# Optimization experiments

Measured on AMD Instinct MI355X. Metric: run time of the kernel, lower is better.

## Reference

```python
import jax, jax.numpy as jnp
import numpy as np
from jax import lax

B, T, C_IN, C_OUT, H = 2048, 128, 2, 16, 232


def setup_inputs() -> dict:
    key = jax.random.key(0)
    k0, k1, k2, k3 = jax.random.split(key, 4)
    X = jax.random.normal(k0, (B, T, C_IN), dtype=jnp.float32)
    # kaiming_normal init (fan_in mode) as in reset_parameters
    conv_w = jax.random.normal(k1, (C_OUT, C_IN, 3), dtype=jnp.float32) * np.sqrt(2.0 / (C_IN * 3))
    conv_b = jnp.zeros((C_OUT,), dtype=jnp.float32)
    w_ih = jax.random.normal(k2, (3 * H, C_OUT), dtype=jnp.float32) * np.sqrt(2.0 / C_OUT)
    w_hh = jax.random.normal(k3, (3 * H, H), dtype=jnp.float32) * np.sqrt(2.0 / H)
    b_ih = jnp.zeros((3 * H,), dtype=jnp.float32)
    b_hh = jnp.zeros((3 * H,), dtype=jnp.float32)
    return {"X": X, "conv_w": conv_w, "conv_b": conv_b,
            "w_ih": w_ih, "w_hh": w_hh, "b_ih": b_ih, "b_hh": b_hh}


def reference(X, conv_w, conv_b, w_ih, w_hh, b_ih, b_hh):
    # Conv1d(2->16, k=3, pad=1) on [B, C, T] + ReLU
    Xc = jnp.transpose(X, (0, 2, 1))                      # [B, 2, T]
    y = lax.conv_general_dilated(Xc, conv_w, window_strides=(1,),
                                 padding=[(1, 1)],
                                 dimension_numbers=("NCH", "OIH", "NCH"))
    y = jax.nn.relu(y + conv_b[None, :, None])            # [B, 16, T]
    x_embed = jnp.transpose(y, (0, 2, 1))                 # [B, T, 16]

    # GRU (torch gate order: r, z, n). Precompute input projections for all t.
    gi = jnp.einsum("btc,gc->btg", x_embed, w_ih) + b_ih  # [B, T, 3H]

    def step(h, g_t):
        gh = h @ w_hh.T + b_hh                            # [B, 3H]
        ir, iz, in_ = jnp.split(g_t, 3, axis=-1)
        hr, hz, hn = jnp.split(gh, 3, axis=-1)
        r = jax.nn.sigmoid(ir + hr)
        z = jax.nn.sigmoid(iz + hz)
        n = jnp.tanh(in_ + r * hn)
        h_new = (1.0 - z) * n + z * h
        return h_new, None

    h0 = jnp.zeros((X.shape[0], w_hh.shape[1]), dtype=X.dtype)
    hT, _ = lax.scan(step, h0, jnp.moveaxis(gi, 1, 0))    # final state [B, H]
    return hT
```

## Files before the change

kernel.cpp:

```cpp
#include <hip/hip_runtime.h>

#define BATCH 2048
#define T     128
#define CIN   2
#define COUT  16
#define H     232
#define RPB   8
#define NBLK  (BATCH/RPB)
#define NTHR  512
#define NGRP  15
#define NT2   48
#define NS    9
#define HROW  272
#define HBUF_H (RPB * HROW)

#define OFF_HA   0
#define SZ_HA    (2 * RPB * HROW * 2)
#define OFF_XE   (OFF_HA + SZ_HA)
#define SZ_XE    (T * RPB * 16 * 2)
#define OFF_WL   (OFF_XE + SZ_XE)
#define SZ_WL    (8 * 14 * 64 * 8 * 2)
#define OFF_CW   (OFF_WL + SZ_WL)
#define SZ_CW    512
#define SMEM_BYTES (OFF_CW + SZ_CW)
#define OFF_XE_H (OFF_XE / 2)

typedef _Float16 half8 __attribute__((ext_vector_type(8)));
typedef float  floatx4 __attribute__((ext_vector_type(4)));

#define MFMA __builtin_amdgcn_mfma_f32_16x16x32_f16

__device__ __align__(16) _Float16 g_packedW[NT2 * NS * 64 * 8];

__global__ void pack_w_kernel(const float* __restrict__ w_ih,
                              const float* __restrict__ w_hh) {
  int tile = blockIdx.x, slice = blockIdx.y, lane = threadIdx.x;
  int grp = tile / NGRP;
  int j   = (tile % NGRP) * 16 + (lane & 15);
  int g   = grp * H + j;
  bool valid = (tile < 3 * NGRP) && (j < H);
  half8 v = {};
  if (valid) {
#pragma unroll
    for (int i = 0; i < 8; ++i) {
      int k = slice * 32 + ((lane >> 4) << 3) + i;
      float f = 0.f;
      if (slice < 8) {
        if (k < H) f = w_hh[g * H + k];
        else if (k < H + COUT && grp < 2) f = w_ih[g * COUT + (k - H)];
      } else {
        int xk = k - 256;
        if (xk >= 0 && xk < COUT && grp == 2) f = w_ih[g * COUT + xk];
      }
      v[i] = (_Float16)f;
    }
  }
  *(half8*)&g_packedW[((tile * NS + slice) * 64 + lane) * 8] = v;
}

__device__ __forceinline__ float sigmoid_f(float x) {
  return __builtin_amdgcn_rcpf(1.f + __expf(-x));
}

__global__ __launch_bounds__(NTHR, 2) void st_gru_kernel(
    const float* __restrict__ X,
    const float* __restrict__ conv_w, const float* __restrict__ conv_b,
    const float* __restrict__ b_ih, const float* __restrict__ b_hh,
    float* __restrict__ out) {

  extern __shared__ __align__(16) char smem[];
  _Float16* lds16  = (_Float16*)smem;
  _Float16* hAflat = (_Float16*)(smem + OFF_HA);
  _Float16* Xemb   = (_Float16*)(smem + OFF_XE);
  _Float16* wLDS   = (_Float16*)(smem + OFF_WL);
  float*    cwp    = (float*)(smem + OFF_CW);

  const int tid  = threadIdx.x;
  const int lane = tid & 63;
  const int wave = tid >> 6;
  const int r_a  = lane & 15;
  const int ch4  = lane >> 4;
  const int blk  = blockIdx.x;
  const int rr   = r_a & 7;
  const int swz  = rr & 3;

  for (int i = tid; i < 2 * RPB * HROW; i += NTHR) hAflat[i] = (_Float16)0;
  if (tid < COUT * CIN * 3) cwp[tid] = conv_w[tid];
  if (tid < COUT) cwp[96 + tid] = conv_b[tid];
  __syncthreads();

  for (int p = tid; p < RPB * T; p += NTHR) {
    int r = p >> 7, t = p & (T - 1);
    const float* xr = X + (size_t)(blk * RPB + r) * (T * CIN);
    float x0[3], x1[3];
#pragma unroll
    for (int d = 0; d < 3; ++d) {
      int tt = t + d - 1;
      bool ok = (unsigned)tt < (unsigned)T;
      x0[d] = ok ? xr[tt * 2] : 0.f;
      x1[d] = ok ? xr[tt * 2 + 1] : 0.f;
    }
    half8 lo, hi;
#pragma unroll
    for (int c = 0; c < COUT; ++c) {
      float a = cwp[96 + c];
#pragma unroll
      for (int d = 0; d < 3; ++d)
        a += x0[d] * cwp[c * 6 + d] + x1[d] * cwp[c * 6 + 3 + d];
      _Float16 hv = (_Float16)fmaxf(a, 0.f);
      if (c < 8) lo[c] = hv; else hi[c - 8] = hv;
    }
    *(half8*)&Xemb[(t * RPB + r) * 16] = lo;
    *(half8*)&Xemb[(t * RPB + r) * 16 + 8] = hi;
  }

  const int gi0 = wave * 2, gi1 = wave * 2 + 1;
  const bool g1ok = (gi1 < NGRP);
  const int tr0 = gi0, tz0 = gi0 + NGRP, tn0 = gi0 + 2 * NGRP;
  const int tr1 = g1ok ? gi1 : 45, tz1 = g1ok ? gi1 + NGRP : 46, tn1 = g1ok ? gi1 + 2 * NGRP : 47;
  const half8* Wp = (const half8*)g_packedW;

  half8* myz = (half8*)(wLDS + wave * (14 * 64 * 8));
#pragma unroll
  for (int f = 0; f < 6; ++f) myz[f * 64 + lane] = Wp[(tz0 * NS + f) * 64 + lane];
#pragma unroll
  for (int f = 0; f < 6; ++f) myz[(6 + f) * 64 + lane] = Wp[(tz1 * NS + f) * 64 + lane];
  myz[12 * 64 + lane] = Wp[(tn0 * NS + 8) * 64 + lane];
  myz[13 * 64 + lane] = Wp[(tn1 * NS + 8) * 64 + lane];

  half8 wr0[8], wr1[8], wn0[8], wn1[8], wzh0[2], wzh1[2];
#pragma unroll
  for (int s = 0; s < 8; ++s) {
    wr0[s] = Wp[(tr0 * NS + s) * 64 + lane];
    wr1[s] = Wp[(tr1 * NS + s) * 64 + lane];
    wn0[s] = Wp[(tn0 * NS + s) * 64 + lane];
    wn1[s] = Wp[(tn1 * NS + s) * 64 + lane];
  }
  wzh0[0] = Wp[(tz0 * NS + 6) * 64 + lane];
  wzh0[1] = Wp[(tz0 * NS + 7) * 64 + lane];
  wzh1[0] = Wp[(tz1 * NS + 6) * 64 + lane];
  wzh1[1] = Wp[(tz1 * NS + 7) * 64 + lane];

  const int j0 = gi0 * 16 + r_a, j1 = gi1 * 16 + r_a;
  float bsr0 = 0.f, bsz0 = 0.f, bin0 = 0.f, bhn0 = 0.f;
  float bsr1 = 0.f, bsz1 = 0.f, bin1 = 0.f, bhn1 = 0.f;
  if (j0 < H) {
    bsr0 = b_ih[j0] + b_hh[j0];
    bsz0 = b_ih[H + j0] + b_hh[H + j0];
    bin0 = b_ih[2 * H + j0]; bhn0 = b_hh[2 * H + j0];
  }
  if (g1ok && j1 < H) {
    bsr1 = b_ih[j1] + b_hh[j1];
    bsz1 = b_ih[H + j1] + b_hh[H + j1];
    bin1 = b_ih[2 * H + j1]; bhn1 = b_hh[2 * H + j1];
  }

  const int eb   = (ch4 & 2);
  const int rowb = ((ch4 & 1) << 2) | (ch4 & 2);

  int woff0[2], woff1[2];
#pragma unroll
  for (int u = 0; u < 2; ++u) {
    int row = rowb + u;
    woff0[u] = row * HROW + ((j0 & ~31) | ((((j0 >> 3) & 3) ^ (row & 3)) << 3) | (j0 & 7));
    woff1[u] = row * HROW + ((j1 & ~31) | ((((j1 >> 3) & 3) ^ (row & 3)) << 3) | (j1 & 7));
  }

  float h0[2] = {0.f, 0.f};
  float h1[2] = {0.f, 0.f};

  const int aoff = rr * HROW + ((ch4 ^ swz) << 3);
  const int inc7 = (ch4 == 0) ? 0 : 256;
  int pa7_e = (ch4 == 0) ? (0      + rr * HROW + 224 + (swz << 3))
                         : (OFF_XE_H + rr * 16 + ((ch4 == 2) ? 8 : 0));
  int pa7_o = (ch4 == 0) ? (HBUF_H + rr * HROW + 224 + (swz << 3))
                         : (OFF_XE_H + 128 + rr * 16 + ((ch4 == 2) ? 8 : 0));
  int a8i = OFF_XE_H + rr * 16 + ((ch4 & 1) << 3);

  __syncthreads();

#define GRU_STEP(RBH, WBH, PA7, A8I) do {                                      \
    half8 A_[7];                                                               \
    _Pragma("unroll")                                                          \
    for (int s = 0; s < 7; ++s)                                                \
      A_[s] = *(const half8*)&lds16[(RBH) + aoff + s * 32];                    \
    half8 A7_ = *(const half8*)&lds16[(PA7)];                                  \
    half8 A8_ = *(const half8*)&lds16[(A8I)];                                  \
    floatx4 ra0 = {}, za0 = {}, na0 = {}, xa0 = {};                            \
    _Pragma("unroll")                                                          \
    for (int s = 0; s < 6; ++s) {                                              \
      ra0 = MFMA(A_[s], wr0[s], ra0, 0, 0, 0);                                 \
      za0 = MFMA(A_[s], myz[s * 64 + lane], za0, 0, 0, 0);                     \
      na0 = MFMA(A_[s], wn0[s], na0, 0, 0, 0);                                 \
    }                                                                          \
    ra0 = MFMA(A_[6], wr0[6], ra0, 0, 0, 0);                                   \
    za0 = MFMA(A_[6], wzh0[0], za0, 0, 0, 0);                                  \
    na0 = MFMA(A_[6], wn0[6], na0, 0, 0, 0);                                   \
    ra0 = MFMA(A7_, wr0[7], ra0, 0, 0, 0);                                     \
    za0 = MFMA(A7_, wzh0[1], za0, 0, 0, 0);                                    \
    na0 = MFMA(A7_, wn0[7], na0, 0, 0, 0);                                     \
    xa0 = MFMA(A8_, myz[12 * 64 + lane], xa0, 0, 0, 0);                        \
    if (g1ok) {                                                                \
      floatx4 ra1 = {}, za1 = {}, na1 = {}, xa1 = {};                          \
      _Pragma("unroll")                                                        \
      for (int s = 0; s < 4; ++s) {                                            \
        ra1 = MFMA(A_[s], wr1[s], ra1, 0, 0, 0);                               \
        za1 = MFMA(A_[s], myz[(6 + s) * 64 + lane], za1, 0, 0, 0);             \
        na1 = MFMA(A_[s], wn1[s], na1, 0, 0, 0);                               \
      }                                                                        \
      float sr_[2], sz_[2];                                                    \
      _Pragma("unroll")                                                        \
      for (int u = 0; u < 2; ++u) {                                            \
        sr_[u] = sigmoid_f(ra0[eb + u] + bsr0);                                \
        sz_[u] = sigmoid_f(za0[eb + u] + bsz0);                                \
      }                                                                        \
      _Pragma("unroll")                                                        \
      for (int s = 4; s < 6; ++s) {                                            \
        ra1 = MFMA(A_[s], wr1[s], ra1, 0, 0, 0);                               \
        za1 = MFMA(A_[s], myz[(6 + s) * 64 + lane], za1, 0, 0, 0);             \
        na1 = MFMA(A_[s], wn1[s], na1, 0, 0, 0);                               \
      }                                                                        \
      ra1 = MFMA(A_[6], wr1[6], ra1, 0, 0, 0);                                 \
      za1 = MFMA(A_[6], wzh1[0], za1, 0, 0, 0);                                \
      na1 = MFMA(A_[6], wn1[6], na1, 0, 0, 0);                                 \
      _Pragma("unroll")                                                        \
      for (int u = 0; u < 2; ++u) {                                            \
        float pre = xa0[eb + u] + bin0 + sr_[u] * (na0[eb + u] + bhn0);        \
        float ee = __expf(2.f * pre);                                          \
        float n = 1.f - 2.f * __builtin_amdgcn_rcpf(ee + 1.f);                 \
        h0[u] = n + sz_[u] * (h0[u] - n);                                      \
        lds16[(WBH) + woff0[u]] = (_Float16)h0[u];                             \
      }                                                                        \
      ra1 = MFMA(A7_, wr1[7], ra1, 0, 0, 0);                                   \
      za1 = MFMA(A7_, wzh1[1], za1, 0, 0, 0);                                  \
      na1 = MFMA(A7_, wn1[7], na1, 0, 0, 0);                                   \
      xa1 = MFMA(A8_, myz[13 * 64 + lane], xa1, 0, 0, 0);                      \
      _Pragma("unroll")                                                        \
      for (int u = 0; u < 2; ++u) {                                            \
        float r = sigmoid_f(ra1[eb + u] + bsr1);                               \
        float z = sigmoid_f(za1[eb + u] + bsz1);                               \
        float pre = xa1[eb + u] + bin1 + r * (na1[eb + u] + bhn1);             \
        float ee = __expf(2.f * pre);                                          \
        float n = 1.f - 2.f * __builtin_amdgcn_rcpf(ee + 1.f);                 \
        h1[u] = n + z * (h1[u] - n);                                           \
        lds16[(WBH) + woff1[u]] = (_Float16)h1[u];                             \
      }                                                                        \
    } else {                                                                   \
      _Pragma("unroll")                                                        \
      for (int u = 0; u < 2; ++u) {                                            \
        float r = sigmoid_f(ra0[eb + u] + bsr0);                               \
        float z = sigmoid_f(za0[eb + u] + bsz0);                               \
        float pre = xa0[eb + u] + bin0 + r * (na0[eb + u] + bhn0);             \
        float ee = __expf(2.f * pre);                                          \
        float n = 1.f - 2.f * __builtin_amdgcn_rcpf(ee + 1.f);                 \
        h0[u] = n + z * (h0[u] - n);                                           \
        lds16[(WBH) + woff0[u]] = (_Float16)h0[u];                             \
      }                                                                        \
    }                                                                          \
    __syncthreads();                                                           \
  } while (0)

  for (int tt = 0; tt < T; tt += 2) {
    GRU_STEP(0,      HBUF_H, pa7_e, a8i);
    GRU_STEP(HBUF_H, 0,      pa7_o, a8i + 128);
    pa7_e += inc7; pa7_o += inc7; a8i += 256;
  }
#undef GRU_STEP

#pragma unroll
  for (int u = 0; u < 2; ++u) {
    int row = rowb + u;
    if (j0 < H) out[(size_t)(blk * RPB + row) * H + j0] = h0[u];
    if (g1ok && j1 < H) out[(size_t)(blk * RPB + row) * H + j1] = h1[u];
  }
}

extern "C" void kernel_launch(void* const* d_in, const int* in_sizes, int n_in,
                              void* d_out, int out_size, void* d_ws, size_t ws_size,
                              hipStream_t stream) {
  const float* X      = (const float*)d_in[0];
  const float* conv_w = (const float*)d_in[1];
  const float* conv_b = (const float*)d_in[2];
  const float* w_ih   = (const float*)d_in[3];
  const float* w_hh   = (const float*)d_in[4];
  const float* b_ih   = (const float*)d_in[5];
  const float* b_hh   = (const float*)d_in[6];
  float* out = (float*)d_out;

  static bool attr_set = false;
  if (!attr_set) {
    hipFuncSetAttribute((const void*)st_gru_kernel,
                        hipFuncAttributeMaxDynamicSharedMemorySize, SMEM_BYTES);
    attr_set = true;
  }

  pack_w_kernel<<<dim3(NT2, NS), 64, 0, stream>>>(w_ih, w_hh);
  st_gru_kernel<<<NBLK, NTHR, SMEM_BYTES, stream>>>(X, conv_w, conv_b, b_ih, b_hh, out);
}
```

Baseline: 185.7 us.

## Reorder GRU step MFMAs into phases and use exp2-based gate activations

```diff
diff --git a/kernel.cpp b/kernel.cpp
--- a/kernel.cpp
+++ b/kernel.cpp
@@ -25,10 +25,14 @@
 #define SMEM_BYTES (OFF_CW + SZ_CW)
 #define OFF_XE_H (OFF_XE / 2)
 
+#define L2E   1.4426950408889634f
+#define TWO_L2E 2.8853900817779268f
+
 typedef _Float16 half8 __attribute__((ext_vector_type(8)));
 typedef float  floatx4 __attribute__((ext_vector_type(4)));
 
 #define MFMA __builtin_amdgcn_mfma_f32_16x16x32_f16
+#define SBAR0() __builtin_amdgcn_sched_barrier(0)
 
 __device__ __align__(16) _Float16 g_packedW[NT2 * NS * 64 * 8];
 
@@ -58,10 +62,6 @@
   *(half8*)&g_packedW[((tile * NS + slice) * 64 + lane) * 8] = v;
 }
 
-__device__ __forceinline__ float sigmoid_f(float x) {
-  return __builtin_amdgcn_rcpf(1.f + __expf(-x));
-}
-
 __global__ __launch_bounds__(NTHR, 2) void st_gru_kernel(
     const float* __restrict__ X,
     const float* __restrict__ conv_w, const float* __restrict__ conv_b,
@@ -142,16 +142,16 @@
   wzh1[1] = Wp[(tz1 * NS + 7) * 64 + lane];
 
   const int j0 = gi0 * 16 + r_a, j1 = gi1 * 16 + r_a;
-  float bsr0 = 0.f, bsz0 = 0.f, bin0 = 0.f, bhn0 = 0.f;
-  float bsr1 = 0.f, bsz1 = 0.f, bin1 = 0.f, bhn1 = 0.f;
+  float nbsr0 = 0.f, nbsz0 = 0.f, bin0 = 0.f, bhn0 = 0.f;
+  float nbsr1 = 0.f, nbsz1 = 0.f, bin1 = 0.f, bhn1 = 0.f;
   if (j0 < H) {
-    bsr0 = b_ih[j0] + b_hh[j0];
-    bsz0 = b_ih[H + j0] + b_hh[H + j0];
+    nbsr0 = -L2E * (b_ih[j0] + b_hh[j0]);
+    nbsz0 = -L2E * (b_ih[H + j0] + b_hh[H + j0]);
     bin0 = b_ih[2 * H + j0]; bhn0 = b_hh[2 * H + j0];
   }
   if (g1ok && j1 < H) {
-    bsr1 = b_ih[j1] + b_hh[j1];
-    bsz1 = b_ih[H + j1] + b_hh[H + j1];
+    nbsr1 = -L2E * (b_ih[j1] + b_hh[j1]);
+    nbsz1 = -L2E * (b_ih[H + j1] + b_hh[H + j1]);
     bin1 = b_ih[2 * H + j1]; bhn1 = b_hh[2 * H + j1];
   }
 
@@ -186,75 +186,72 @@
       A_[s] = *(const half8*)&lds16[(RBH) + aoff + s * 32];                    \
     half8 A7_ = *(const half8*)&lds16[(PA7)];                                  \
     half8 A8_ = *(const half8*)&lds16[(A8I)];                                  \
-    floatx4 ra0 = {}, za0 = {}, na0 = {}, xa0 = {};                            \
-    _Pragma("unroll")                                                          \
-    for (int s = 0; s < 6; ++s) {                                              \
+      \
+    floatx4 ra0 = {}, na0 = {}, za0 = {}, ra1 = {}, na1 = {}, za1 = {};        \
+    _Pragma("unroll")                                                          \
+    for (int s = 0; s < 7; ++s) {                                              \
       ra0 = MFMA(A_[s], wr0[s], ra0, 0, 0, 0);                                 \
-      za0 = MFMA(A_[s], myz[s * 64 + lane], za0, 0, 0, 0);                     \
       na0 = MFMA(A_[s], wn0[s], na0, 0, 0, 0);                                 \
-    }                                                                          \
-    ra0 = MFMA(A_[6], wr0[6], ra0, 0, 0, 0);                                   \
-    za0 = MFMA(A_[6], wzh0[0], za0, 0, 0, 0);                                  \
-    na0 = MFMA(A_[6], wn0[6], na0, 0, 0, 0);                                   \
-    ra0 = MFMA(A7_, wr0[7], ra0, 0, 0, 0);                                     \
-    za0 = MFMA(A7_, wzh0[1], za0, 0, 0, 0);                                    \
-    na0 = MFMA(A7_, wn0[7], na0, 0, 0, 0);                                     \
-    xa0 = MFMA(A8_, myz[12 * 64 + lane], xa0, 0, 0, 0);                        \
-    if (g1ok) {                                                                \
-      floatx4 ra1 = {}, za1 = {}, na1 = {}, xa1 = {};                          \
-      _Pragma("unroll")                                                        \
-      for (int s = 0; s < 4; ++s) {                                            \
+      if (g1ok) {                                                              \
         ra1 = MFMA(A_[s], wr1[s], ra1, 0, 0, 0);                               \
-        za1 = MFMA(A_[s], myz[(6 + s) * 64 + lane], za1, 0, 0, 0);             \
         na1 = MFMA(A_[s], wn1[s], na1, 0, 0, 0);                               \
       }                                                                        \
-      float sr_[2], sz_[2];                                                    \
+    }                                                                          \
+    za0 = MFMA(A_[6], wzh0[0], za0, 0, 0, 0);                                  \
+    za0 = MFMA(A7_, wzh0[1], za0, 0, 0, 0);                                    \
+    ra0 = MFMA(A7_, wr0[7], ra0, 0, 0, 0);                                     \
+    na0 = MFMA(A7_, wn0[7], na0, 0, 0, 0);                                     \
+    if (g1ok) {                                                                \
+      za1 = MFMA(A_[6], wzh1[0], za1, 0, 0, 0);                                \
+      za1 = MFMA(A7_, wzh1[1], za1, 0, 0, 0);                                  \
+      ra1 = MFMA(A7_, wr1[7], ra1, 0, 0, 0);                                   \
+      na1 = MFMA(A7_, wn1[7], na1, 0, 0, 0);                                   \
+    }                                                                          \
+       \
+    float sr0_[2], sr1_[2];                                                    \
+    _Pragma("unroll")                                                          \
+    for (int u = 0; u < 2; ++u) {                                              \
+      sr0_[u] = __builtin_amdgcn_rcpf(                                         \
+          1.f + __builtin_amdgcn_exp2f(fmaf(ra0[eb + u], -L2E, nbsr0)));       \
+      sr1_[u] = __builtin_amdgcn_rcpf(                                         \
+          1.f + __builtin_amdgcn_exp2f(fmaf(ra1[eb + u], -L2E, nbsr1)));       \
+    }                                                                          \
+    SBAR0();                                                                   \
+                        \
+    floatx4 xa0 = {};                                                          \
+    _Pragma("unroll")                                                          \
+    for (int s = 0; s < 6; ++s)                                                \
+      za0 = MFMA(A_[s], myz[s * 64 + lane], za0, 0, 0, 0);                     \
+    xa0 = MFMA(A8_, myz[12 * 64 + lane], xa0, 0, 0, 0);                        \
+                                   \
+    _Pragma("unroll")                                                          \
+    for (int u = 0; u < 2; ++u) {                                              \
+      float sz = __builtin_amdgcn_rcpf(                                        \
+          1.f + __builtin_amdgcn_exp2f(fmaf(za0[eb + u], -L2E, nbsz0)));       \
+      float pre = fmaf(sr0_[u], na0[eb + u] + bhn0, xa0[eb + u] + bin0);       \
+      float e2 = __builtin_amdgcn_exp2f(pre * TWO_L2E);                        \
+      float n = fmaf(-2.f, __builtin_amdgcn_rcpf(e2 + 1.f), 1.f);              \
+      h0[u] = fmaf(sz, h0[u] - n, n);                                          \
+      lds16[(WBH) + woff0[u]] = (_Float16)h0[u];                               \
+    }                                                                          \
+    SBAR0();                                                                   \
+                        \
+    if (g1ok) {                                                                \
+      floatx4 xa1 = {};                                                        \
+      _Pragma("unroll")                                                        \
+      for (int s = 0; s < 6; ++s)                                              \
+        za1 = MFMA(A_[s], myz[(6 + s) * 64 + lane], za1, 0, 0, 0);             \
+      xa1 = MFMA(A8_, myz[13 * 64 + lane], xa1, 0, 0, 0);                      \
+                                          \
       _Pragma("unroll")                                                        \
       for (int u = 0; u < 2; ++u) {                                            \
-        sr_[u] = sigmoid_f(ra0[eb + u] + bsr0);                                \
-        sz_[u] = sigmoid_f(za0[eb + u] + bsz0);                                \
-      }                                                                        \
-      _Pragma("unroll")                                                        \
-      for (int s = 4; s < 6; ++s) {                                            \
-        ra1 = MFMA(A_[s], wr1[s], ra1, 0, 0, 0);                               \
-        za1 = MFMA(A_[s], myz[(6 + s) * 64 + lane], za1, 0, 0, 0);             \
-        na1 = MFMA(A_[s], wn1[s], na1, 0, 0, 0);                               \
-      }                                                                        \
-      ra1 = MFMA(A_[6], wr1[6], ra1, 0, 0, 0);                                 \
-      za1 = MFMA(A_[6], wzh1[0], za1, 0, 0, 0);                                \
-      na1 = MFMA(A_[6], wn1[6], na1, 0, 0, 0);                                 \
-      _Pragma("unroll")                                                        \
-      for (int u = 0; u < 2; ++u) {                                            \
-        float pre = xa0[eb + u] + bin0 + sr_[u] * (na0[eb + u] + bhn0);        \
-        float ee = __expf(2.f * pre);                                          \
-        float n = 1.f - 2.f * __builtin_amdgcn_rcpf(ee + 1.f);                 \
-        h0[u] = n + sz_[u] * (h0[u] - n);                                      \
-        lds16[(WBH) + woff0[u]] = (_Float16)h0[u];                             \
-      }                                                                        \
-      ra1 = MFMA(A7_, wr1[7], ra1, 0, 0, 0);                                   \
-      za1 = MFMA(A7_, wzh1[1], za1, 0, 0, 0);                                  \
-      na1 = MFMA(A7_, wn1[7], na1, 0, 0, 0);                                   \
-      xa1 = MFMA(A8_, myz[13 * 64 + lane], xa1, 0, 0, 0);                      \
-      _Pragma("unroll")                                                        \
-      for (int u = 0; u < 2; ++u) {                                            \
-        float r = sigmoid_f(ra1[eb + u] + bsr1);                               \
-        float z = sigmoid_f(za1[eb + u] + bsz1);                               \
-        float pre = xa1[eb + u] + bin1 + r * (na1[eb + u] + bhn1);             \
-        float ee = __expf(2.f * pre);                                          \
-        float n = 1.f - 2.f * __builtin_amdgcn_rcpf(ee + 1.f);                 \
-        h1[u] = n + z * (h1[u] - n);                                           \
+        float sz = __builtin_amdgcn_rcpf(                                      \
+            1.f + __builtin_amdgcn_exp2f(fmaf(za1[eb + u], -L2E, nbsz1)));     \
+        float pre = fmaf(sr1_[u], na1[eb + u] + bhn1, xa1[eb + u] + bin1);     \
+        float e2 = __builtin_amdgcn_exp2f(pre * TWO_L2E);                      \
+        float n = fmaf(-2.f, __builtin_amdgcn_rcpf(e2 + 1.f), 1.f);            \
+        h1[u] = fmaf(sz, h1[u] - n, n);                                        \
         lds16[(WBH) + woff1[u]] = (_Float16)h1[u];                             \
-      }                                                                        \
-    } else {                                                                   \
-      _Pragma("unroll")                                                        \
-      for (int u = 0; u < 2; ++u) {                                            \
-        float r = sigmoid_f(ra0[eb + u] + bsr0);                               \
-        float z = sigmoid_f(za0[eb + u] + bsz0);                               \
-        float pre = xa0[eb + u] + bin0 + r * (na0[eb + u] + bhn0);             \
-        float ee = __expf(2.f * pre);                                          \
-        float n = 1.f - 2.f * __builtin_amdgcn_rcpf(ee + 1.f);                 \
-        h0[u] = n + z * (h0[u] - n);                                           \
-        lds16[(WBH) + woff0[u]] = (_Float16)h0[u];                             \
       }                                                                        \
     }                                                                          \
     __syncthreads();                                                           \
```

After: 195.9 us. 1.05x slower.

## Move more z-gate weights to registers, use exp2 with folded biases, add wave priority

Applied to the files above, without the earlier changes.

```diff
diff --git a/kernel.cpp b/kernel.cpp
--- a/kernel.cpp
+++ b/kernel.cpp
@@ -19,16 +19,20 @@
 #define OFF_XE   (OFF_HA + SZ_HA)
 #define SZ_XE    (T * RPB * 16 * 2)
 #define OFF_WL   (OFF_XE + SZ_XE)
-#define SZ_WL    (8 * 14 * 64 * 8 * 2)
+#define SZ_WL    (8 * 10 * 64 * 8 * 2)
 #define OFF_CW   (OFF_WL + SZ_WL)
 #define SZ_CW    512
 #define SMEM_BYTES (OFF_CW + SZ_CW)
 #define OFF_XE_H (OFF_XE / 2)
 
+#define L2E     1.4426950408889634f
+#define TWO_L2E 2.8853900817779268f
+
 typedef _Float16 half8 __attribute__((ext_vector_type(8)));
 typedef float  floatx4 __attribute__((ext_vector_type(4)));
 
 #define MFMA __builtin_amdgcn_mfma_f32_16x16x32_f16
+#define PRIO(n) __builtin_amdgcn_s_setprio(n)
 
 __device__ __align__(16) _Float16 g_packedW[NT2 * NS * 64 * 8];
 
@@ -58,10 +62,6 @@
   *(half8*)&g_packedW[((tile * NS + slice) * 64 + lane) * 8] = v;
 }
 
-__device__ __forceinline__ float sigmoid_f(float x) {
-  return __builtin_amdgcn_rcpf(1.f + __expf(-x));
-}
-
 __global__ __launch_bounds__(NTHR, 2) void st_gru_kernel(
     const float* __restrict__ X,
     const float* __restrict__ conv_w, const float* __restrict__ conv_b,
@@ -120,15 +120,15 @@
   const int tr1 = g1ok ? gi1 : 45, tz1 = g1ok ? gi1 + NGRP : 46, tn1 = g1ok ? gi1 + 2 * NGRP : 47;
   const half8* Wp = (const half8*)g_packedW;
 
-  half8* myz = (half8*)(wLDS + wave * (14 * 64 * 8));
-#pragma unroll
-  for (int f = 0; f < 6; ++f) myz[f * 64 + lane] = Wp[(tz0 * NS + f) * 64 + lane];
-#pragma unroll
-  for (int f = 0; f < 6; ++f) myz[(6 + f) * 64 + lane] = Wp[(tz1 * NS + f) * 64 + lane];
-  myz[12 * 64 + lane] = Wp[(tn0 * NS + 8) * 64 + lane];
-  myz[13 * 64 + lane] = Wp[(tn1 * NS + 8) * 64 + lane];
-
-  half8 wr0[8], wr1[8], wn0[8], wn1[8], wzh0[2], wzh1[2];
+  half8* myz = (half8*)(wLDS + wave * (10 * 64 * 8));
+#pragma unroll
+  for (int f = 0; f < 4; ++f) myz[f * 64 + lane] = Wp[(tz0 * NS + f) * 64 + lane];
+#pragma unroll
+  for (int f = 0; f < 4; ++f) myz[(4 + f) * 64 + lane] = Wp[(tz1 * NS + f) * 64 + lane];
+  myz[8 * 64 + lane] = Wp[(tn0 * NS + 8) * 64 + lane];
+  myz[9 * 64 + lane] = Wp[(tn1 * NS + 8) * 64 + lane];
+
+  half8 wr0[8], wr1[8], wn0[8], wn1[8], wzh0[4], wzh1[4];
 #pragma unroll
   for (int s = 0; s < 8; ++s) {
     wr0[s] = Wp[(tr0 * NS + s) * 64 + lane];
@@ -136,22 +136,23 @@
     wn0[s] = Wp[(tn0 * NS + s) * 64 + lane];
     wn1[s] = Wp[(tn1 * NS + s) * 64 + lane];
   }
-  wzh0[0] = Wp[(tz0 * NS + 6) * 64 + lane];
-  wzh0[1] = Wp[(tz0 * NS + 7) * 64 + lane];
-  wzh1[0] = Wp[(tz1 * NS + 6) * 64 + lane];
-  wzh1[1] = Wp[(tz1 * NS + 7) * 64 + lane];
+#pragma unroll
+  for (int s = 0; s < 4; ++s) {
+    wzh0[s] = Wp[(tz0 * NS + 4 + s) * 64 + lane];
+    wzh1[s] = Wp[(tz1 * NS + 4 + s) * 64 + lane];
+  }
 
   const int j0 = gi0 * 16 + r_a, j1 = gi1 * 16 + r_a;
-  float bsr0 = 0.f, bsz0 = 0.f, bin0 = 0.f, bhn0 = 0.f;
-  float bsr1 = 0.f, bsz1 = 0.f, bin1 = 0.f, bhn1 = 0.f;
+  float nbsr0 = 0.f, nbsz0 = 0.f, bin0 = 0.f, bhn0 = 0.f;
+  float nbsr1 = 0.f, nbsz1 = 0.f, bin1 = 0.f, bhn1 = 0.f;
   if (j0 < H) {
-    bsr0 = b_ih[j0] + b_hh[j0];
-    bsz0 = b_ih[H + j0] + b_hh[H + j0];
+    nbsr0 = -L2E * (b_ih[j0] + b_hh[j0]);
+    nbsz0 = -L2E * (b_ih[H + j0] + b_hh[H + j0]);
     bin0 = b_ih[2 * H + j0]; bhn0 = b_hh[2 * H + j0];
   }
   if (g1ok && j1 < H) {
-    bsr1 = b_ih[j1] + b_hh[j1];
-    bsz1 = b_ih[H + j1] + b_hh[H + j1];
+    nbsr1 = -L2E * (b_ih[j1] + b_hh[j1]);
+    nbsz1 = -L2E * (b_ih[H + j1] + b_hh[H + j1]);
     bin1 = b_ih[2 * H + j1]; bhn1 = b_hh[2 * H + j1];
   }
 
@@ -186,74 +187,93 @@
       A_[s] = *(const half8*)&lds16[(RBH) + aoff + s * 32];                    \
     half8 A7_ = *(const half8*)&lds16[(PA7)];                                  \
     half8 A8_ = *(const half8*)&lds16[(A8I)];                                  \
+    PRIO(1);                                                                   \
+                 \
     floatx4 ra0 = {}, za0 = {}, na0 = {}, xa0 = {};                            \
     _Pragma("unroll")                                                          \
-    for (int s = 0; s < 6; ++s) {                                              \
+    for (int s = 0; s < 4; ++s) {                                              \
       ra0 = MFMA(A_[s], wr0[s], ra0, 0, 0, 0);                                 \
       za0 = MFMA(A_[s], myz[s * 64 + lane], za0, 0, 0, 0);                     \
       na0 = MFMA(A_[s], wn0[s], na0, 0, 0, 0);                                 \
     }                                                                          \
-    ra0 = MFMA(A_[6], wr0[6], ra0, 0, 0, 0);                                   \
-    za0 = MFMA(A_[6], wzh0[0], za0, 0, 0, 0);                                  \
-    na0 = MFMA(A_[6], wn0[6], na0, 0, 0, 0);                                   \
+    _Pragma("unroll")                                                          \
+    for (int s = 4; s < 7; ++s) {                                              \
+      ra0 = MFMA(A_[s], wr0[s], ra0, 0, 0, 0);                                 \
+      za0 = MFMA(A_[s], wzh0[s - 4], za0, 0, 0, 0);                            \
+      na0 = MFMA(A_[s], wn0[s], na0, 0, 0, 0);                                 \
+    }                                                                          \
     ra0 = MFMA(A7_, wr0[7], ra0, 0, 0, 0);                                     \
-    za0 = MFMA(A7_, wzh0[1], za0, 0, 0, 0);                                    \
+    za0 = MFMA(A7_, wzh0[3], za0, 0, 0, 0);                                    \
     na0 = MFMA(A7_, wn0[7], na0, 0, 0, 0);                                     \
-    xa0 = MFMA(A8_, myz[12 * 64 + lane], xa0, 0, 0, 0);                        \
+    xa0 = MFMA(A8_, myz[8 * 64 + lane], xa0, 0, 0, 0);                         \
     if (g1ok) {                                                                \
+                                       \
       floatx4 ra1 = {}, za1 = {}, na1 = {}, xa1 = {};                          \
       _Pragma("unroll")                                                        \
       for (int s = 0; s < 4; ++s) {                                            \
         ra1 = MFMA(A_[s], wr1[s], ra1, 0, 0, 0);                               \
-        za1 = MFMA(A_[s], myz[(6 + s) * 64 + lane], za1, 0, 0, 0);             \
+        za1 = MFMA(A_[s], myz[(4 + s) * 64 + lane], za1, 0, 0, 0);             \
         na1 = MFMA(A_[s], wn1[s], na1, 0, 0, 0);                               \
       }                                                                        \
+      PRIO(0);                                                                 \
+                      \
       float sr_[2], sz_[2];                                                    \
       _Pragma("unroll")                                                        \
       for (int u = 0; u < 2; ++u) {                                            \
-        sr_[u] = sigmoid_f(ra0[eb + u] + bsr0);                                \
-        sz_[u] = sigmoid_f(za0[eb + u] + bsz0);                                \
-      }                                                                        \
-      _Pragma("unroll")                                                        \
-      for (int s = 4; s < 6; ++s) {                                            \
+        sr_[u] = __builtin_amdgcn_rcpf(                                        \
+            1.f + __builtin_amdgcn_exp2f(fmaf(ra0[eb + u], -L2E, nbsr0)));     \
+        sz_[u] = __builtin_amdgcn_rcpf(                                        \
+            1.f + __builtin_amdgcn_exp2f(fmaf(za0[eb + u], -L2E, nbsz0)));     \
+      }                                                                        \
+      PRIO(1);                                                                 \
+      _Pragma("unroll")                                                        \
+      for (int s = 4; s < 7; ++s) {                                            \
         ra1 = MFMA(A_[s], wr1[s], ra1, 0, 0, 0);                               \
-        za1 = MFMA(A_[s], myz[(6 + s) * 64 + lane], za1, 0, 0, 0);             \
+        za1 = MFMA(A_[s], wzh1[s - 4], za1, 0, 0, 0);                          \
         na1 = MFMA(A_[s], wn1[s], na1, 0, 0, 0);                               \
       }                                                                        \
-      ra1 = MFMA(A_[6], wr1[6], ra1, 0, 0, 0);                                 \
-      za1 = MFMA(A_[6], wzh1[0], za1, 0, 0, 0);                                \
-      na1 = MFMA(A_[6], wn1[6], na1, 0, 0, 0);                                 \
+      PRIO(0);                                                                 \
+                                        \
       _Pragma("unroll")                                                        \
       for (int u = 0; u < 2; ++u) {                                            \
-        float pre = xa0[eb + u] + bin0 + sr_[u] * (na0[eb + u] + bhn0);        \
-        float ee = __expf(2.f * pre);                                          \
-        float n = 1.f - 2.f * __builtin_amdgcn_rcpf(ee + 1.f);                 \
-        h0[u] = n + sz_[u] * (h0[u] - n);                                      \
+        float pre = fmaf(sr_[u], na0[eb + u] + bhn0, xa0[eb + u] + bin0);      \
+        float e2 = __builtin_amdgcn_exp2f(pre * TWO_L2E);                      \
+        float n = fmaf(-2.f, __builtin_amdgcn_rcpf(e2 + 1.f), 1.f);            \
+        h0[u] = fmaf(sz_[u], h0[u] - n, n);                                    \
         lds16[(WBH) + woff0[u]] = (_Float16)h0[u];                             \
       }                                                                        \
+      PRIO(1);                                                                 \
       ra1 = MFMA(A7_, wr1[7], ra1, 0, 0, 0);                                   \
-      za1 = MFMA(A7_, wzh1[1], za1, 0, 0, 0);                                  \
+      za1 = MFMA(A7_, wzh1[3], za1, 0, 0, 0);                                  \
       na1 = MFMA(A7_, wn1[7], na1, 0, 0, 0);                                   \
-      xa1 = MFMA(A8_, myz[13 * 64 + lane], xa1, 0, 0, 0);                      \
+      xa1 = MFMA(A8_, myz[9 * 64 + lane], xa1, 0, 0, 0);                       \
+      PRIO(0);                                                                 \
+                                                                 \
       _Pragma("unroll")                                                        \
       for (int u = 0; u < 2; ++u) {                                            \
-        float r = sigmoid_f(ra1[eb + u] + bsr1);                               \
-        float z = sigmoid_f(za1[eb + u] + bsz1);                               \
-        float pre = xa1[eb + u] + bin1 + r * (na1[eb + u] + bhn1);             \
-        float ee = __expf(2.f * pre);                                          \
-        float n = 1.f - 2.f * __builtin_amdgcn_rcpf(ee + 1.f);                 \
-        h1[u] = n + z * (h1[u] - n);                                           \
+        float r = __builtin_amdgcn_rcpf(                                       \
+            1.f + __builtin_amdgcn_exp2f(fmaf(ra1[eb + u], -L2E, nbsr1)));     \
+        float z = __builtin_amdgcn_rcpf(                                       \
+            1.f + __builtin_amdgcn_exp2f(fmaf(za1[eb + u], -L2E, nbsz1)));     \
+        float pre = fmaf(r, na1[eb + u] + bhn1, xa1[eb + u] + bin1);           \
+        float e2 = __builtin_amdgcn_exp2f(pre * TWO_L2E);                      \
+        float n = fmaf(-2.f, __builtin_amdgcn_rcpf(e2 + 1.f), 1.f);            \
+        h1[u] = fmaf(z, h1[u] - n, n);                                         \
         lds16[(WBH) + woff1[u]] = (_Float16)h1[u];                             \
       }                                                                        \
     } else {                                                                   \
+      PRIO(0);                                                                 \
+                                             \
       _Pragma("unroll")                                                        \
       for (int u = 0; u < 2; ++u) {                                            \
-        float r = sigmoid_f(ra0[eb + u] + bsr0);                               \
-        float z = sigmoid_f(za0[eb + u] + bsz0);                               \
-        float pre = xa0[eb + u] + bin0 + r * (na0[eb + u] + bhn0);             \
-        float ee = __expf(2.f * pre);                                          \
-        float n = 1.f - 2.f * __builtin_amdgcn_rcpf(ee + 1.f);                 \
-        h0[u] = n + z * (h0[u] - n);                                           \
+        float r = __builtin_amdgcn_rcpf(                                       \
+            1.f + __builtin_amdgcn_exp2f(fmaf(ra0[eb + u], -L2E, nbsr0)));     \
+        float z = __builtin_amdgcn_rcpf(                                       \
+            1.f + __builtin_amdgcn_exp2f(fmaf(za0[eb + u], -L2E, nbsz0)));     \
+        float pre = fmaf(r, na0[eb + u] + bhn0, xa0[eb + u] + bin0);           \
+        float e2 = __builtin_amdgcn_exp2f(pre * TWO_L2E);                      \
+        float n = fmaf(-2.f, __builtin_amdgcn_rcpf(e2 + 1.f), 1.f);            \
+        h0[u] = fmaf(z, h0[u] - n, n);                                         \
         lds16[(WBH) + woff0[u]] = (_Float16)h0[u];                             \
       }                                                                        \
     }                                                                          \
```

Result: slower. 223.2 us (+20.2%).
